# Kernel optimization log

Measured on AMD Instinct MI355X. Metric: run time of the kernel, lower is better.

The kernel has to match this reference:

```python
import jax, jax.numpy as jnp
import numpy as np

B, S, H = 2, 1024, 4096
NH, NKV, HD = 32, 8, 128
THETA = 10000.0
NEG = -1e9


def ternary_quant(w):
    # BitNet b1.58 absmean ternary weight quantization (dequantized math).
    gamma = jnp.mean(jnp.abs(w)) + 1e-5
    wq = jnp.clip(jnp.round(w / gamma), -1.0, 1.0) * gamma
    # straight-through estimator for gradients
    return w + jax.lax.stop_gradient(wq - w)


def rope_cos_sin(position_ids):
    # position_ids: (B, S) int -> cos/sin (B, S, HD)
    inv_freq = 1.0 / (THETA ** (jnp.arange(0, HD, 2, dtype=jnp.float32) / HD))
    freqs = position_ids.astype(jnp.float32)[..., None] * inv_freq  # (B,S,HD/2)
    emb = jnp.concatenate([freqs, freqs], axis=-1)  # (B,S,HD)
    return jnp.cos(emb), jnp.sin(emb)


def rotate_half(x):
    x1, x2 = x[..., : HD // 2], x[..., HD // 2 :]
    return jnp.concatenate([-x2, x1], axis=-1)


def setup_inputs() -> dict:
    key = jax.random.key(0)
    k0, k1, k2, k3, k4 = jax.random.split(key, 5)
    hidden_states = jax.random.normal(k0, (B, S, H), dtype=jnp.float32)
    # torch Linear weight layout: (out_features, in_features)
    Wq = jax.random.normal(k1, (NH * HD, H), dtype=jnp.float32) * 0.02
    Wk = jax.random.normal(k2, (NKV * HD, H), dtype=jnp.float32) * 0.02
    Wv = jax.random.normal(k3, (NKV * HD, H), dtype=jnp.float32) * 0.02
    Wo = jax.random.normal(k4, (H, NH * HD), dtype=jnp.float32) * 0.02
    # additive causal mask (B,1,S,S): 0 where allowed, -1e9 where j > i
    causal = jnp.tril(jnp.ones((S, S), dtype=bool))
    attention_mask = jnp.where(causal, 0.0, NEG).astype(jnp.float32)
    attention_mask = jnp.broadcast_to(attention_mask[None, None], (B, 1, S, S))
    position_ids = jnp.broadcast_to(jnp.arange(S, dtype=jnp.int32)[None], (B, S))
    return {
        "hidden_states": hidden_states,
        "Wq": Wq, "Wk": Wk, "Wv": Wv, "Wo": Wo,
        "attention_mask": attention_mask,
        "position_ids": position_ids,
    }


def reference(hidden_states, Wq, Wk, Wv, Wo, attention_mask, position_ids):
    # quantized projections (BitNet ternary weights, dequantized matmul)
    q = jnp.einsum("bsh,oh->bso", hidden_states, ternary_quant(Wq))
    k = jnp.einsum("bsh,oh->bso", hidden_states, ternary_quant(Wk))
    v = jnp.einsum("bsh,oh->bso", hidden_states, ternary_quant(Wv))

    q = q.reshape(B, S, NH, HD).transpose(0, 2, 1, 3)    # (B,NH,S,HD)
    k = k.reshape(B, S, NKV, HD).transpose(0, 2, 1, 3)   # (B,NKV,S,HD)
    v = v.reshape(B, S, NKV, HD).transpose(0, 2, 1, 3)

    cos, sin = rope_cos_sin(position_ids)                # (B,S,HD)
    cos, sin = cos[:, None], sin[:, None]                # (B,1,S,HD)
    q = q * cos + rotate_half(q) * sin
    k = k * cos + rotate_half(k) * sin

    # GQA: repeat kv heads
    rep = NH // NKV
    k = jnp.repeat(k, rep, axis=1)                       # (B,NH,S,HD)
    v = jnp.repeat(v, rep, axis=1)

    scores = jnp.einsum("bhqd,bhkd->bhqk", q, k) / jnp.sqrt(
        jnp.asarray(HD, dtype=q.dtype))
    scores = scores + attention_mask
    attn = jax.nn.softmax(scores, axis=-1)
    out = jnp.einsum("bhqk,bhkd->bhqd", attn, v)         # (B,NH,S,HD)
    out = out.transpose(0, 2, 1, 3).reshape(B, S, NH * HD)
    out = jnp.einsum("bso,ho->bsh", out, ternary_quant(Wo))
    return out
```

## Files before the change

kernel.cpp:

```cpp
#include <hip/hip_runtime.h>
#include <hip/hip_bf16.h>

using short8 = __attribute__((ext_vector_type(8))) short;
using f32x4  = __attribute__((ext_vector_type(4))) float;

#define B_   2
#define S_   1024
#define H_   4096
#define NH_  32
#define NKV_ 8
#define HD_  128
#define MROWS 2048
#define SCALE_ 0.08838834764831845f

__device__ __forceinline__ ushort f2bf(float x) {
    uint32_t u = __float_as_uint(x);
    uint32_t r = (u + 0x7FFFu + ((u >> 16) & 1u)) >> 16;
    return (ushort)r;
}

__device__ __forceinline__ void gload16(const void* g, void* l) {
    __builtin_amdgcn_global_load_lds((const __attribute__((address_space(1))) void*)g,
                                     (__attribute__((address_space(3))) void*)l, 16, 0, 0);
}

__global__ void k_abssum(const float* __restrict__ w, int n, float* __restrict__ out) {
    __shared__ float red[256];
    float s = 0.f;
    int i = blockIdx.x * blockDim.x + threadIdx.x;
    int stride = gridDim.x * blockDim.x;
    const float4* w4 = (const float4*)w;
    int n4 = n >> 2;
    for (int j = i; j < n4; j += stride) {
        float4 v = w4[j];
        s += fabsf(v.x) + fabsf(v.y) + fabsf(v.z) + fabsf(v.w);
    }
    red[threadIdx.x] = s;
    __syncthreads();
    for (int off = 128; off > 0; off >>= 1) {
        if ((int)threadIdx.x < off) red[threadIdx.x] += red[threadIdx.x + off];
        __syncthreads();
    }
    if (threadIdx.x == 0) atomicAdd(out, red[0]);
}

__global__ void k_quant(const float* __restrict__ w, int n, const float* __restrict__ sump,
                        float inv_n, ushort* __restrict__ t) {
    float gamma = sump[0] * inv_n + 1e-5f;
    int i = blockIdx.x * blockDim.x + threadIdx.x;
    int stride = gridDim.x * blockDim.x;
    int n4 = n >> 2;
    const float4* w4 = (const float4*)w;
    ushort4* t4 = (ushort4*)t;
    for (int j = i; j < n4; j += stride) {
        float4 v = w4[j];
        ushort4 o;
        o.x = f2bf(fminf(fmaxf(rintf(v.x / gamma), -1.f), 1.f));
        o.y = f2bf(fminf(fmaxf(rintf(v.y / gamma), -1.f), 1.f));
        o.z = f2bf(fminf(fmaxf(rintf(v.z / gamma), -1.f), 1.f));
        o.w = f2bf(fminf(fmaxf(rintf(v.w / gamma), -1.f), 1.f));
        t4[j] = o;
    }
}

__global__ void k_cast(const float* __restrict__ x, int n4, ushort* __restrict__ y) {
    int i = blockIdx.x * blockDim.x + threadIdx.x;
    int stride = gridDim.x * blockDim.x;
    const float4* x4 = (const float4*)x;
    ushort4* y4 = (ushort4*)y;
    for (int j = i; j < n4; j += stride) {
        float4 v = x4[j];
        ushort4 o;
        o.x = f2bf(v.x); o.y = f2bf(v.y); o.z = f2bf(v.z); o.w = f2bf(v.w);
        y4[j] = o;
    }
}

__global__ void k_rope_table(const int* __restrict__ pos, float* __restrict__ cost,
                             float* __restrict__ sint) {
    int idx = blockIdx.x * blockDim.x + threadIdx.x;
    if (idx >= B_ * S_ * 64) return;
    int d = idx & 63;
    int bs = idx >> 6;
    float p = (float)pos[bs];
    float inv_freq = powf(10000.0f, -(float)d * (1.0f / 64.0f));
    float f = p * inv_freq;
    float sn, cs;
    __sincosf(f, &sn, &cs);
    cs = cosf(f);
    sn = sinf(f);
    cost[idx] = cs;
    sint[idx] = sn;
}

__global__ void k_rope_pack(const float* __restrict__ src, const float* __restrict__ cost,
                            const float* __restrict__ sint, ushort* __restrict__ dst,
                            int nheads, int total) {
    int idx = blockIdx.x * blockDim.x + threadIdx.x;
    if (idx >= total) return;
    int d = idx & 63;
    int h = (idx >> 6) % nheads;
    int bs = idx / (64 * nheads);
    int s = bs & (S_ - 1);
    int b = bs >> 10;
    float c = cost[bs * 64 + d];
    float sn = sint[bs * 64 + d];
    const float* sp = src + (size_t)bs * (nheads * 128) + h * 128 + d;
    float x1 = sp[0], x2 = sp[64];
    ushort* dp = dst + (((size_t)(b * nheads + h)) * S_ + s) * HD_ + d;
    dp[0]  = f2bf(x1 * c - x2 * sn);
    dp[64] = f2bf(x2 * c + x1 * sn);
}

__global__ void k_vt(const float* __restrict__ v, ushort* __restrict__ vt) {
    int bid = blockIdx.x;
    int st = bid & 31;
    int dt = (bid >> 5) & 3;
    int bh = bid >> 7;
    int b = bh >> 3, hk = bh & 7;
    __shared__ float tile[32][33];
    int tx = threadIdx.x & 31, ty = threadIdx.x >> 5;
    #pragma unroll
    for (int i = 0; i < 4; ++i) {
        int srow = st * 32 + ty + i * 8;
        tile[ty + i * 8][tx] = v[((size_t)(b * S_ + srow)) * (NKV_ * HD_) + hk * 128 + dt * 32 + tx];
    }
    __syncthreads();
    #pragma unroll
    for (int i = 0; i < 4; ++i) {
        int d = dt * 32 + ty + i * 8;
        vt[((size_t)((b * 8 + hk) * 128 + d)) * S_ + st * 32 + tx] = f2bf(tile[tx][ty + i * 8]);
    }
}

__device__ __forceinline__ void gemm_tile_nt(const ushort* __restrict__ A,
                                             const ushort* __restrict__ Bw,
                                             float* __restrict__ C, int ldc, int K,
                                             int mbase, int nbase, float gamma,
                                             ushort* lA, ushort* lB) {
    int tid = threadIdx.x;
    int lane = tid & 63, w = tid >> 6;
    int wr = w >> 1, wc = w & 1;
    f32x4 acc[4][4];
    #pragma unroll
    for (int i = 0; i < 4; ++i)
        #pragma unroll
        for (int j = 0; j < 4; ++j) acc[i][j] = (f32x4){0.f, 0.f, 0.f, 0.f};

    int c0 = tid, c1 = tid + 256;
    const ushort* ga0 = A + ((size_t)(mbase + (c0 >> 2))) * K + (c0 & 3) * 8;
    const ushort* ga1 = A + ((size_t)(mbase + (c1 >> 2))) * K + (c1 & 3) * 8;
    const ushort* gb0 = Bw + ((size_t)(nbase + (c0 >> 2))) * K + (c0 & 3) * 8;
    const ushort* gb1 = Bw + ((size_t)(nbase + (c1 >> 2))) * K + (c1 & 3) * 8;

    int rb = wr * 64 + (lane & 15);
    int cb = wc * 64 + (lane & 15);
    int ko = (lane >> 4) * 8;

    for (int k0 = 0; k0 < K; k0 += 32) {
        gload16(ga0 + k0, lA + c0 * 8);
        gload16(ga1 + k0, lA + c1 * 8);
        gload16(gb0 + k0, lB + c0 * 8);
        gload16(gb1 + k0, lB + c1 * 8);
        __syncthreads();
        short8 af[4], bfr[4];
        #pragma unroll
        for (int i = 0; i < 4; ++i) af[i]  = *(const short8*)&lA[(rb + i * 16) * 32 + ko];
        #pragma unroll
        for (int j = 0; j < 4; ++j) bfr[j] = *(const short8*)&lB[(cb + j * 16) * 32 + ko];
        #pragma unroll
        for (int i = 0; i < 4; ++i)
            #pragma unroll
            for (int j = 0; j < 4; ++j)
                acc[i][j] = __builtin_amdgcn_mfma_f32_16x16x32_bf16(af[i], bfr[j], acc[i][j], 0, 0, 0);
        __syncthreads();
    }
    int r0 = mbase + wr * 64 + (lane >> 4) * 4;
    int cg = nbase + wc * 64 + (lane & 15);
    #pragma unroll
    for (int i = 0; i < 4; ++i)
        #pragma unroll
        for (int j = 0; j < 4; ++j)
            #pragma unroll
            for (int r = 0; r < 4; ++r)
                C[(size_t)(r0 + i * 16 + r) * ldc + cg + j * 16] = gamma * acc[i][j][r];
}

__global__ __launch_bounds__(256) void k_gemm_qkv(const ushort* __restrict__ hsb,
                                                  const ushort* __restrict__ Tq,
                                                  const ushort* __restrict__ Tk,
                                                  const ushort* __restrict__ Tv,
                                                  const float* __restrict__ sums,
                                                  float* __restrict__ qb_,
                                                  float* __restrict__ kb_,
                                                  float* __restrict__ vb_) {
    __shared__ ushort lA[128 * 32];
    __shared__ ushort lB[128 * 32];
    int bid = blockIdx.x;
    int mt = bid & 15, ntg = bid >> 4;
    const ushort* Bw; float* C; int ldc, nt; float gamma;
    if (ntg < 32)      { Bw = Tq; C = qb_; ldc = 4096; nt = ntg;      gamma = sums[0] * (1.f / 16777216.f) + 1e-5f; }
    else if (ntg < 40) { Bw = Tk; C = kb_; ldc = 1024; nt = ntg - 32; gamma = sums[1] * (1.f / 4194304.f)  + 1e-5f; }
    else               { Bw = Tv; C = vb_; ldc = 1024; nt = ntg - 40; gamma = sums[2] * (1.f / 4194304.f)  + 1e-5f; }
    gemm_tile_nt(hsb, Bw, C, ldc, 4096, mt * 128, nt * 128, gamma, lA, lB);
}

__global__ __launch_bounds__(256) void k_gemm_out(const ushort* __restrict__ ao,
                                                  const ushort* __restrict__ To,
                                                  const float* __restrict__ sums,
                                                  float* __restrict__ out) {
    __shared__ ushort lA[128 * 32];
    __shared__ ushort lB[128 * 32];
    int mt = blockIdx.x & 15, nt = blockIdx.x >> 4;
    float gamma = sums[3] * (1.f / 16777216.f) + 1e-5f;
    gemm_tile_nt(ao, To, out, 4096, 4096, mt * 128, nt * 128, gamma, lA, lB);
}

__global__ __launch_bounds__(64) void k_attn(const ushort* __restrict__ qr,
                                             const ushort* __restrict__ kr,
                                             const ushort* __restrict__ vt,
                                             ushort* __restrict__ ao) {
    int bid = blockIdx.x;
    int qt = bid & 63;
    int h  = (bid >> 6) & 31;
    int b  = bid >> 11;
    int hk = h >> 2;
    int l  = threadIdx.x;
    int lm = l & 15, lg = l >> 4;
    int qb = qt * 16;
    __shared__ ushort pl[16 * 32];

    const ushort* qp = qr + (((size_t)(b * NH_ + h)) * S_ + qb + lm) * HD_ + lg * 8;
    short8 qf[4];
    #pragma unroll
    for (int f = 0; f < 4; ++f) qf[f] = *(const short8*)(qp + f * 32);

    f32x4 acc[8];
    #pragma unroll
    for (int f = 0; f < 8; ++f) acc[f] = (f32x4){0.f, 0.f, 0.f, 0.f};
    float mr[4] = {-1e30f, -1e30f, -1e30f, -1e30f};
    float lr[4] = {0.f, 0.f, 0.f, 0.f};

    const ushort* kbp = kr + ((size_t)(b * NKV_ + hk)) * S_ * HD_;
    const ushort* vbp = vt + ((size_t)(b * NKV_ + hk)) * HD_ * S_;

    int nkt = (qb + 47) >> 5;
    for (int kt = 0; kt < nkt; ++kt) {
        int kb = kt * 32;
        f32x4 sc[2];
        #pragma unroll
        for (int sub = 0; sub < 2; ++sub) {
            sc[sub] = (f32x4){0.f, 0.f, 0.f, 0.f};
            const ushort* kp = kbp + (size_t)(kb + sub * 16 + lm) * HD_ + lg * 8;
            #pragma unroll
            for (int f = 0; f < 4; ++f) {
                short8 kf = *(const short8*)(kp + f * 32);
                sc[sub] = __builtin_amdgcn_mfma_f32_16x16x32_bf16(qf[f], kf, sc[sub], 0, 0, 0);
            }
        }
        float pmax[4] = {-1e30f, -1e30f, -1e30f, -1e30f};
        #pragma unroll
        for (int sub = 0; sub < 2; ++sub)
            #pragma unroll
            for (int r = 0; r < 4; ++r) {
                int kidx = kb + sub * 16 + lm;
                int qidx = qb + lg * 4 + r;
                float sv = sc[sub][r] * SCALE_;
                if (kidx > qidx) sv = -1e30f;
                sc[sub][r] = sv;
                pmax[r] = fmaxf(pmax[r], sv);
            }
        #pragma unroll
        for (int r = 0; r < 4; ++r) {
            #pragma unroll
            for (int off = 1; off < 16; off <<= 1)
                pmax[r] = fmaxf(pmax[r], __shfl_xor(pmax[r], off));
        }
        float corr[4], rsum[4];
        #pragma unroll
        for (int r = 0; r < 4; ++r) {
            float Mn = fmaxf(mr[r], pmax[r]);
            corr[r] = __expf(mr[r] - Mn);
            mr[r] = Mn;
            rsum[r] = 0.f;
        }
        #pragma unroll
        for (int sub = 0; sub < 2; ++sub)
            #pragma unroll
            for (int r = 0; r < 4; ++r) {
                float p = __expf(sc[sub][r] - mr[r]);
                rsum[r] += p;
                pl[(lg * 4 + r) * 32 + sub * 16 + lm] = f2bf(p);
            }
        #pragma unroll
        for (int r = 0; r < 4; ++r) {
            #pragma unroll
            for (int off = 1; off < 16; off <<= 1)
                rsum[r] += __shfl_xor(rsum[r], off);
            lr[r] = lr[r] * corr[r] + rsum[r];
        }
        #pragma unroll
        for (int f = 0; f < 8; ++f)
            #pragma unroll
            for (int r = 0; r < 4; ++r) acc[f][r] *= corr[r];
        __syncthreads();
        short8 pa = *(const short8*)&pl[lm * 32 + lg * 8];
        #pragma unroll
        for (int f = 0; f < 8; ++f) {
            short8 vf = *(const short8*)&vbp[(size_t)(f * 16 + lm) * S_ + kb + lg * 8];
            acc[f] = __builtin_amdgcn_mfma_f32_16x16x32_bf16(pa, vf, acc[f], 0, 0, 0);
        }
        __syncthreads();
    }
    #pragma unroll
    for (int f = 0; f < 8; ++f) {
        int d = f * 16 + lm;
        #pragma unroll
        for (int r = 0; r < 4; ++r) {
            int s = qb + lg * 4 + r;
            ao[((size_t)(b * S_) + s) * (NH_ * HD_) + h * HD_ + d] = f2bf(acc[f][r] / lr[r]);
        }
    }
}

extern "C" void kernel_launch(void* const* d_in, const int* in_sizes, int n_in,
                              void* d_out, int out_size, void* d_ws, size_t ws_size,
                              hipStream_t stream) {
    (void)in_sizes; (void)n_in; (void)out_size; (void)ws_size;
    const float* hs = (const float*)d_in[0];
    const float* Wq = (const float*)d_in[1];
    const float* Wk = (const float*)d_in[2];
    const float* Wv = (const float*)d_in[3];
    const float* Wo = (const float*)d_in[4];
    const int* pos = (const int*)d_in[6];
    float* out = (float*)d_out;

    char* ws = (char*)d_ws;
    size_t off = 0;
    auto alloc = [&](size_t bytes) -> void* {
        void* p = ws + off;
        off += (bytes + 255) & ~(size_t)255;
        return p;
    };
    float*  sums = (float*)alloc(256);
    ushort* hsb  = (ushort*)alloc((size_t)MROWS * 4096 * 2);
    ushort* Tq   = (ushort*)alloc((size_t)4096 * 4096 * 2);
    ushort* Tk   = (ushort*)alloc((size_t)1024 * 4096 * 2);
    ushort* Tv   = (ushort*)alloc((size_t)1024 * 4096 * 2);
    ushort* To   = (ushort*)alloc((size_t)4096 * 4096 * 2);
    float*  qb_  = (float*)alloc((size_t)MROWS * 4096 * 4);
    float*  kb_  = (float*)alloc((size_t)MROWS * 1024 * 4);
    float*  vb_  = (float*)alloc((size_t)MROWS * 1024 * 4);
    ushort* qrb  = (ushort*)alloc((size_t)B_ * NH_ * S_ * HD_ * 2);
    ushort* krb  = (ushort*)alloc((size_t)B_ * NKV_ * S_ * HD_ * 2);
    ushort* vtb  = (ushort*)alloc((size_t)B_ * NKV_ * HD_ * S_ * 2);
    float*  cost = (float*)alloc((size_t)B_ * S_ * 64 * 4);
    float*  sint = (float*)alloc((size_t)B_ * S_ * 64 * 4);
    ushort* ao   = (ushort*)alloc((size_t)MROWS * 4096 * 2);

    hipMemsetAsync(sums, 0, 256, stream);
    k_abssum<<<1024, 256, 0, stream>>>(Wq, 16777216, sums + 0);
    k_abssum<<<1024, 256, 0, stream>>>(Wk, 4194304,  sums + 1);
    k_abssum<<<1024, 256, 0, stream>>>(Wv, 4194304,  sums + 2);
    k_abssum<<<1024, 256, 0, stream>>>(Wo, 16777216, sums + 3);
    k_quant<<<2048, 256, 0, stream>>>(Wq, 16777216, sums + 0, 1.f / 16777216.f, Tq);
    k_quant<<<2048, 256, 0, stream>>>(Wk, 4194304,  sums + 1, 1.f / 4194304.f,  Tk);
    k_quant<<<2048, 256, 0, stream>>>(Wv, 4194304,  sums + 2, 1.f / 4194304.f,  Tv);
    k_quant<<<2048, 256, 0, stream>>>(Wo, 16777216, sums + 3, 1.f / 16777216.f, To);
    k_cast<<<2048, 256, 0, stream>>>(hs, (MROWS * 4096) / 4, hsb);
    k_rope_table<<<512, 256, 0, stream>>>(pos, cost, sint);
    k_gemm_qkv<<<16 * 48, 256, 0, stream>>>(hsb, Tq, Tk, Tv, sums, qb_, kb_, vb_);
    k_rope_pack<<<16384, 256, 0, stream>>>(qb_, cost, sint, qrb, NH_,  B_ * S_ * NH_ * 64);
    k_rope_pack<<<4096, 256, 0, stream>>>(kb_, cost, sint, krb, NKV_, B_ * S_ * NKV_ * 64);
    k_vt<<<2048, 256, 0, stream>>>(vb_, vtb);
    k_attn<<<B_ * NH_ * (S_ / 16), 64, 0, stream>>>(qrb, krb, vtb, ao);
    k_gemm_out<<<16 * 32, 256, 0, stream>>>(ao, To, sums, out);
}
```

Baseline: 763.9 us.

## Rewrite attention kernel with 32x32 MFMA, register-only P transfer and lazy rescale

The attention kernel now handles 32 query rows per wavefront using 32x32x16 bf16 MFMA, computing S^T so each lane owns one query column. The probabilities are moved from the score layout to the PV operand layout with cross-half shuffles instead of an LDS round-trip with syncthreads. The online-softmax rescale is skipped unless the running max grows by more than 8, and query tiles are launched in reverse order so the longest causal tiles start first. The grid is halved and each wave does more work, which reduces parallelism but cuts overhead per key tile. A redundant sincos call in the rope table is also removed.

```diff
diff --git a/kernel.cpp b/kernel.cpp
--- a/kernel.cpp
+++ b/kernel.cpp
@@ -3,6 +3,7 @@
 
 using short8 = __attribute__((ext_vector_type(8))) short;
 using f32x4  = __attribute__((ext_vector_type(4))) float;
+using f32x16 = __attribute__((ext_vector_type(16))) float;
 
 #define B_   2
 #define S_   1024
@@ -85,12 +86,8 @@
     float p = (float)pos[bs];
     float inv_freq = powf(10000.0f, -(float)d * (1.0f / 64.0f));
     float f = p * inv_freq;
-    float sn, cs;
-    __sincosf(f, &sn, &cs);
-    cs = cosf(f);
-    sn = sinf(f);
-    cost[idx] = cs;
-    sint[idx] = sn;
+    cost[idx] = cosf(f);
+    sint[idx] = sinf(f);
 }
 
 __global__ void k_rope_pack(const float* __restrict__ src, const float* __restrict__ cost,
@@ -221,105 +218,108 @@
                                              const ushort* __restrict__ vt,
                                              ushort* __restrict__ ao) {
     int bid = blockIdx.x;
-    int qt = bid & 63;
-    int h  = (bid >> 6) & 31;
-    int b  = bid >> 11;
+    int qt = 31 - (bid & 31);
+    int h  = (bid >> 5) & 31;
+    int b  = bid >> 10;
     int hk = h >> 2;
-    int l  = threadIdx.x;
-    int lm = l & 15, lg = l >> 4;
-    int qb = qt * 16;
-    __shared__ ushort pl[16 * 32];
-
-    const ushort* qp = qr + (((size_t)(b * NH_ + h)) * S_ + qb + lm) * HD_ + lg * 8;
-    short8 qf[4];
-    #pragma unroll
-    for (int f = 0; f < 4; ++f) qf[f] = *(const short8*)(qp + f * 32);
-
-    f32x4 acc[8];
-    #pragma unroll
-    for (int f = 0; f < 8; ++f) acc[f] = (f32x4){0.f, 0.f, 0.f, 0.f};
-    float mr[4] = {-1e30f, -1e30f, -1e30f, -1e30f};
-    float lr[4] = {0.f, 0.f, 0.f, 0.f};
-
-    const ushort* kbp = kr + ((size_t)(b * NKV_ + hk)) * S_ * HD_;
-    const ushort* vbp = vt + ((size_t)(b * NKV_ + hk)) * HD_ * S_;
-
-    int nkt = (qb + 47) >> 5;
-    for (int kt = 0; kt < nkt; ++kt) {
-        int kb = kt * 32;
-        f32x4 sc[2];
-        #pragma unroll
-        for (int sub = 0; sub < 2; ++sub) {
-            sc[sub] = (f32x4){0.f, 0.f, 0.f, 0.f};
-            const ushort* kp = kbp + (size_t)(kb + sub * 16 + lm) * HD_ + lg * 8;
+    int lane = threadIdx.x;
+    int qcol = lane & 31;
+    int hi = lane >> 5;
+    int q0 = qt * 32;
+
+    const ushort* qp = qr + (((size_t)(b * NH_ + h)) * S_ + q0 + qcol) * HD_ + hi * 8;
+    short8 qf[8];
+    #pragma unroll
+    for (int dc = 0; dc < 8; ++dc) qf[dc] = *(const short8*)(qp + dc * 16);
+
+    f32x16 acc[4];
+    #pragma unroll
+    for (int i = 0; i < 4; ++i)
+        #pragma unroll
+        for (int r = 0; r < 16; ++r) acc[i][r] = 0.f;
+
+    float m = -1e30f, lsum = 0.f;
+    const ushort* kbase = kr + ((size_t)(b * NKV_ + hk)) * S_ * HD_;
+    const ushort* vbase = vt + ((size_t)(b * NKV_ + hk)) * HD_ * S_;
+
+    int nfull = q0 >> 5;
+    for (int kt = 0; kt <= nfull; ++kt) {
+        int kb = kt << 5;
+        f32x16 sc;
+        #pragma unroll
+        for (int r = 0; r < 16; ++r) sc[r] = 0.f;
+        const ushort* kp = kbase + ((size_t)(kb + qcol)) * HD_ + hi * 8;
+        #pragma unroll
+        for (int dc = 0; dc < 8; ++dc) {
+            short8 kf = *(const short8*)(kp + dc * 16);
+            sc = __builtin_amdgcn_mfma_f32_32x32x16_bf16(kf, qf[dc], sc, 0, 0, 0);
+        }
+        short8 v0f[4], v1f[4];
+        #pragma unroll
+        for (int dblk = 0; dblk < 4; ++dblk) {
+            const ushort* vp = vbase + ((size_t)(dblk * 32 + qcol)) * S_ + kb + hi * 8;
+            v0f[dblk] = *(const short8*)vp;
+            v1f[dblk] = *(const short8*)(vp + 16);
+        }
+        float p[16]; float smax = -1e30f;
+        bool diag = (kt == nfull);
+        #pragma unroll
+        for (int r = 0; r < 16; ++r) {
+            int krow = (r & 3) + 8 * (r >> 2) + 4 * hi;
+            float v = sc[r] * SCALE_;
+            if (diag && krow > qcol) v = -1e30f;
+            p[r] = v;
+            smax = fmaxf(smax, v);
+        }
+        smax = fmaxf(smax, __shfl_xor(smax, 32));
+        if (__any(smax > m + 8.f)) {
+            float mn = fmaxf(m, smax);
+            float corr = __expf(m - mn);
+            m = mn;
+            lsum *= corr;
             #pragma unroll
-            for (int f = 0; f < 4; ++f) {
-                short8 kf = *(const short8*)(kp + f * 32);
-                sc[sub] = __builtin_amdgcn_mfma_f32_16x16x32_bf16(qf[f], kf, sc[sub], 0, 0, 0);
+            for (int r = 0; r < 16; ++r) {
+                float cf = __shfl(corr, (r & 3) + 8 * (r >> 2) + 4 * hi);
+                #pragma unroll
+                for (int i = 0; i < 4; ++i) acc[i][r] *= cf;
             }
         }
-        float pmax[4] = {-1e30f, -1e30f, -1e30f, -1e30f};
-        #pragma unroll
-        for (int sub = 0; sub < 2; ++sub)
-            #pragma unroll
-            for (int r = 0; r < 4; ++r) {
-                int kidx = kb + sub * 16 + lm;
-                int qidx = qb + lg * 4 + r;
-                float sv = sc[sub][r] * SCALE_;
-                if (kidx > qidx) sv = -1e30f;
-                sc[sub][r] = sv;
-                pmax[r] = fmaxf(pmax[r], sv);
-            }
-        #pragma unroll
-        for (int r = 0; r < 4; ++r) {
-            #pragma unroll
-            for (int off = 1; off < 16; off <<= 1)
-                pmax[r] = fmaxf(pmax[r], __shfl_xor(pmax[r], off));
-        }
-        float corr[4], rsum[4];
-        #pragma unroll
-        for (int r = 0; r < 4; ++r) {
-            float Mn = fmaxf(mr[r], pmax[r]);
-            corr[r] = __expf(mr[r] - Mn);
-            mr[r] = Mn;
-            rsum[r] = 0.f;
-        }
-        #pragma unroll
-        for (int sub = 0; sub < 2; ++sub)
-            #pragma unroll
-            for (int r = 0; r < 4; ++r) {
-                float p = __expf(sc[sub][r] - mr[r]);
-                rsum[r] += p;
-                pl[(lg * 4 + r) * 32 + sub * 16 + lm] = f2bf(p);
-            }
-        #pragma unroll
-        for (int r = 0; r < 4; ++r) {
-            #pragma unroll
-            for (int off = 1; off < 16; off <<= 1)
-                rsum[r] += __shfl_xor(rsum[r], off);
-            lr[r] = lr[r] * corr[r] + rsum[r];
-        }
-        #pragma unroll
-        for (int f = 0; f < 8; ++f)
-            #pragma unroll
-            for (int r = 0; r < 4; ++r) acc[f][r] *= corr[r];
-        __syncthreads();
-        short8 pa = *(const short8*)&pl[lm * 32 + lg * 8];
-        #pragma unroll
-        for (int f = 0; f < 8; ++f) {
-            short8 vf = *(const short8*)&vbp[(size_t)(f * 16 + lm) * S_ + kb + lg * 8];
-            acc[f] = __builtin_amdgcn_mfma_f32_16x16x32_bf16(pa, vf, acc[f], 0, 0, 0);
-        }
-        __syncthreads();
-    }
-    #pragma unroll
-    for (int f = 0; f < 8; ++f) {
-        int d = f * 16 + lm;
-        #pragma unroll
-        for (int r = 0; r < 4; ++r) {
-            int s = qb + lg * 4 + r;
-            ao[((size_t)(b * S_) + s) * (NH_ * HD_) + h * HD_ + d] = f2bf(acc[f][r] / lr[r]);
-        }
+        float psum = 0.f;
+        #pragma unroll
+        for (int r = 0; r < 16; ++r) { p[r] = __expf(p[r] - m); psum += p[r]; }
+        psum += __shfl_xor(psum, 32);
+        lsum += psum;
+        unsigned int wd[8], xw[8];
+        #pragma unroll
+        for (int i = 0; i < 8; ++i)
+            wd[i] = (unsigned int)f2bf(p[2 * i]) | ((unsigned int)f2bf(p[2 * i + 1]) << 16);
+        #pragma unroll
+        for (int i = 0; i < 8; ++i) xw[i] = (unsigned int)__shfl_xor((int)wd[i], 32);
+        union U8 { unsigned int u[4]; short8 s; } ua0, ua1;
+        ua0.u[0] = hi ? xw[2] : wd[0];
+        ua0.u[1] = hi ? xw[3] : wd[1];
+        ua0.u[2] = hi ? wd[2] : xw[0];
+        ua0.u[3] = hi ? wd[3] : xw[1];
+        ua1.u[0] = hi ? xw[6] : wd[4];
+        ua1.u[1] = hi ? xw[7] : wd[5];
+        ua1.u[2] = hi ? wd[6] : xw[4];
+        ua1.u[3] = hi ? wd[7] : xw[5];
+        #pragma unroll
+        for (int dblk = 0; dblk < 4; ++dblk) {
+            acc[dblk] = __builtin_amdgcn_mfma_f32_32x32x16_bf16(ua0.s, v0f[dblk], acc[dblk], 0, 0, 0);
+            acc[dblk] = __builtin_amdgcn_mfma_f32_32x32x16_bf16(ua1.s, v1f[dblk], acc[dblk], 0, 0, 0);
+        }
+    }
+    float linv = 1.f / lsum;
+    #pragma unroll
+    for (int r = 0; r < 16; ++r) {
+        int crow = (r & 3) + 8 * (r >> 2) + 4 * hi;
+        float lf = __shfl(linv, crow);
+        int qrow = q0 + crow;
+        ushort* op = ao + ((size_t)(b * S_) + qrow) * (NH_ * HD_) + h * HD_ + qcol;
+        #pragma unroll
+        for (int dblk = 0; dblk < 4; ++dblk)
+            op[dblk * 32] = f2bf(acc[dblk][r] * lf);
     }
 }
 
@@ -373,6 +373,6 @@
     k_rope_pack<<<16384, 256, 0, stream>>>(qb_, cost, sint, qrb, NH_,  B_ * S_ * NH_ * 64);
     k_rope_pack<<<4096, 256, 0, stream>>>(kb_, cost, sint, krb, NKV_, B_ * S_ * NKV_ * 64);
     k_vt<<<2048, 256, 0, stream>>>(vb_, vtb);
-    k_attn<<<B_ * NH_ * (S_ / 16), 64, 0, stream>>>(qrb, krb, vtb, ao);
+    k_attn<<<B_ * NH_ * (S_ / 32), 64, 0, stream>>>(qrb, krb, vtb, ao);
     k_gemm_out<<<16 * 32, 256, 0, stream>>>(ao, To, sums, out);
 }
```

Result: faster. 711.8 us (-6.8%).
